# Kernel optimization log

Hardware: AMD Instinct MI355X
Metric: run time of the kernel (lower is better)

The kernel has to match this reference:

```python
import jax, jax.numpy as jnp
import numpy as np
import math

B, S, HID = 2, 2048, 2048
NH, NKV, HD = 16, 4, 128
ROPE_BASE = 10000.0

def _rope(x, position_ids):
    # x: [B, H, S, HD], position_ids: [B, S]
    half = HD // 2
    inv_freq = 1.0 / (ROPE_BASE ** (jnp.arange(0, half, dtype=jnp.float32) / half))
    freqs = position_ids.astype(jnp.float32)[:, :, None] * inv_freq[None, None, :]  # [B,S,half]
    cos = jnp.cos(freqs)[:, None, :, :]  # [B,1,S,half]
    sin = jnp.sin(freqs)[:, None, :, :]
    x1, x2 = x[..., :half], x[..., half:]
    return jnp.concatenate([x1 * cos - x2 * sin, x2 * cos + x1 * sin], axis=-1)

def setup_inputs() -> dict:
    key = jax.random.key(0)
    k1, k2, k3 = jax.random.split(key, 3)
    x = jax.random.normal(k1, (B, S, HID), dtype=jnp.float32)
    position_ids = jnp.broadcast_to(jnp.arange(S, dtype=jnp.int64 if jax.config.jax_enable_x64 else jnp.int32)[None, :], (B, S))
    causal = jnp.tril(jnp.ones((S, S), dtype=bool))
    mask = jnp.where(causal, 0.0, -1e9).astype(jnp.float32)[None, None, :, :]
    w_qkv = jax.random.normal(k2, (NH * HD + 2 * NKV * HD, HID), dtype=jnp.float32) * 0.02
    w_o = jax.random.normal(k3, (HID, HID), dtype=jnp.float32) * 0.02
    return {"x": x, "position_ids": position_ids, "mask": mask, "w_qkv": w_qkv, "w_o": w_o}

def reference(x, position_ids, mask, w_qkv, w_o):
    qkv = x @ w_qkv.T  # [B,S,3072]
    q_dim, kv_dim = NH * HD, NKV * HD
    q = qkv[..., :q_dim].reshape(B, S, NH, HD).transpose(0, 2, 1, 3)          # [B,NH,S,HD]
    k = qkv[..., q_dim:q_dim + kv_dim].reshape(B, S, NKV, HD).transpose(0, 2, 1, 3)
    v = qkv[..., q_dim + kv_dim:].reshape(B, S, NKV, HD).transpose(0, 2, 1, 3)
    q = _rope(q, position_ids)
    k = _rope(k, position_ids)
    n_rep = NH // NKV
    k = jnp.repeat(k, n_rep, axis=1)  # [B,NH,S,HD]
    v = jnp.repeat(v, n_rep, axis=1)
    scores = jnp.einsum('bhqd,bhkd->bhqk', q, k) / math.sqrt(HD) + mask
    attn = jax.nn.softmax(scores, axis=-1)  # dropout p=0.0 -> identity
    out = jnp.einsum('bhqk,bhkd->bhqd', attn, v)
    out = out.transpose(0, 2, 1, 3).reshape(B, S, HID)
    return out @ w_o.T
```

## Files before the change

kernel.cpp:

```cpp
#include <hip/hip_runtime.h>
#include <hip/hip_bf16.h>
#include <cstdint>
#include <cstddef>

typedef unsigned short u16;
typedef __attribute__((ext_vector_type(8))) __bf16 bf16x8;
typedef __attribute__((ext_vector_type(4))) float floatx4;

#define B_    2
#define S_    2048
#define HID_  2048
#define NH_   16
#define NKV_  4
#define HD_   128
#define QKVN_ 3072

__device__ __forceinline__ float bf2f(u16 u) {
  union { unsigned int i; float f; } v; v.i = ((unsigned int)u) << 16; return v.f;
}
__device__ __forceinline__ u16 f2bf(float f) {
  union { float f; unsigned int i; } v; v.f = f;
  unsigned int u = v.i;
  return (u16)((u + 0x7fffu + ((u >> 16) & 1u)) >> 16);
}

#define GLOAD_LDS16(gp, lp)                                                  \
  __builtin_amdgcn_global_load_lds(                                          \
      (__attribute__((address_space(1))) void*)(gp),                         \
      (__attribute__((address_space(3))) void*)(lp), 16, 0, 0)

__global__ __launch_bounds__(256)
void cast_f32_bf16(const float* __restrict__ in, u16* __restrict__ out, int n)
{
  const int i = (blockIdx.x * 256 + threadIdx.x) * 8;
  if (i >= n) return;
  const float4 a = *(const float4*)(in + i);
  const float4 b = *(const float4*)(in + i + 4);
  union { u16 h[8]; uint4 v; } o;
  o.h[0] = f2bf(a.x); o.h[1] = f2bf(a.y); o.h[2] = f2bf(a.z); o.h[3] = f2bf(a.w);
  o.h[4] = f2bf(b.x); o.h[5] = f2bf(b.y); o.h[6] = f2bf(b.z); o.h[7] = f2bf(b.w);
  *(uint4*)(out + i) = o.v;
}

template <bool F32OUT>
__global__ __launch_bounds__(256, 2)
void gemm_bt_128(const u16* __restrict__ A, const u16* __restrict__ W,
                 void* __restrict__ Cv, int N, int K, int lda, int ldc)
{
  __shared__ __align__(16) u16 lA[128 * 64];
  __shared__ __align__(16) u16 lB[128 * 64];
  const int tid  = threadIdx.x;
  const int w    = tid >> 6, ln = tid & 63;
  const int quad = ln >> 4,  l15 = ln & 15;
  const int m0 = blockIdx.y * 128, n0 = blockIdx.x * 128;
  const int waveM = (w >> 1) * 64, waveN = (w & 1) * 64;

  const floatx4 vzero = {0.f, 0.f, 0.f, 0.f};
  floatx4 acc[4][4];
#pragma unroll
  for (int i = 0; i < 4; ++i)
#pragma unroll
    for (int j = 0; j < 4; ++j) acc[i][j] = vzero;

  for (int k0 = 0; k0 < K; k0 += 64) {
    __syncthreads();
#pragma unroll
    for (int p = 0; p < 4; ++p) {
      const int L = (p * 4 + w) * 64 + ln;
      const int row = L >> 3, c = L & 7;
      GLOAD_LDS16(A + (size_t)(m0 + row) * lda + k0 + c * 8, lA + L * 8);
      GLOAD_LDS16(W + (size_t)(n0 + row) * K   + k0 + c * 8, lB + L * 8);
    }
    __syncthreads();
#pragma unroll
    for (int kk = 0; kk < 64; kk += 32) {
      bf16x8 aF[4], bF[4];
      const int cbase = (kk >> 3) + quad;
#pragma unroll
      for (int t = 0; t < 4; ++t) {
        const int rowA = waveM + t * 16 + l15;
        aF[t] = *(const bf16x8*)(lA + rowA * 64 + cbase * 8);
        const int rowB = waveN + t * 16 + l15;
        bF[t] = *(const bf16x8*)(lB + rowB * 64 + cbase * 8);
      }
#pragma unroll
      for (int i = 0; i < 4; ++i)
#pragma unroll
        for (int j = 0; j < 4; ++j)
          acc[i][j] = __builtin_amdgcn_mfma_f32_16x16x32_bf16(aF[i], bF[j], acc[i][j], 0, 0, 0);
    }
  }
#pragma unroll
  for (int i = 0; i < 4; ++i)
#pragma unroll
    for (int r = 0; r < 4; ++r) {
      const int row = m0 + waveM + i * 16 + quad * 4 + r;
      if (F32OUT) {
        float* cp = (float*)Cv + (size_t)row * ldc + n0 + waveN + l15;
#pragma unroll
        for (int j = 0; j < 4; ++j) cp[j * 16] = acc[i][j][r];
      } else {
        u16* cp = (u16*)Cv + (size_t)row * ldc + n0 + waveN + l15;
#pragma unroll
        for (int j = 0; j < 4; ++j) cp[j * 16] = f2bf(acc[i][j][r]);
      }
    }
}

__global__ __launch_bounds__(256)
void rope_inplace(u16* __restrict__ qkv, u16* __restrict__ vt_ws)
{
  const int s = blockIdx.x, b = blockIdx.y;
  const int tid = threadIdx.x;
  __shared__ float cs[64], sn[64];
  if (tid < 64) {
    const float inv = powf(10000.0f, -((float)tid) / 64.0f);
    float s_, c_;
    sincosf((float)s * inv, &s_, &c_);
    cs[tid] = c_; sn[tid] = s_;
  }
  __syncthreads();
  u16* base = qkv + ((size_t)b * S_ + s) * QKVN_;
  for (int p = tid; p < NH_ * 64; p += 256) {
    const int h = p >> 6, i = p & 63;
    u16* hp = base + h * 128;
    const float x1 = bf2f(hp[i]);
    const float x2 = bf2f(hp[64 + i]);
    hp[i]      = f2bf(x1 * cs[i] - x2 * sn[i]);
    hp[64 + i] = f2bf(x2 * cs[i] + x1 * sn[i]);
  }
  for (int p = tid; p < NKV_ * 64; p += 256) {
    const int h = p >> 6, i = p & 63;
    u16* hp = base + NH_ * HD_ + h * 128;
    const float x1 = bf2f(hp[i]);
    const float x2 = bf2f(hp[64 + i]);
    hp[i]      = f2bf(x1 * cs[i] - x2 * sn[i]);
    hp[64 + i] = f2bf(x2 * cs[i] + x1 * sn[i]);
  }
  for (int p = tid; p < NKV_ * HD_; p += 256) {
    const int h = p >> 7, d = p & 127;
    vt_ws[((size_t)(b * NKV_ + h) * HD_ + d) * S_ + s] =
        base[NH_ * HD_ + NKV_ * HD_ + h * 128 + d];
  }
}

#define LPP 68
#define KSLOT(key, s) ((key) * 128 + (((s) ^ ((key) & 7)) * 8))
#define VSLOT(d, s)   ((d) * 64  + (((s) ^ ((d) & 7)) * 8))

__global__ __launch_bounds__(256, 2)
void flash_attn(u16* __restrict__ qkv, const u16* __restrict__ vt_ws)
{
  const int pi = blockIdx.x;
  const int h  = blockIdx.y;
  const int b  = blockIdx.z;
  const int tid  = threadIdx.x;
  const int w    = tid >> 6, ln = tid & 63;
  const int quad = ln >> 4,  l15 = ln & 15;
  const int kvh  = h >> 2;

  const int qtA = 31 - pi, qtB = pi;
  const int itA = qtA + 1;
  const int nIt = itA + qtB + 1;

  __shared__ __align__(16) u16 lK[2][64 * 128];
  __shared__ __align__(16) u16 lVt[2][128 * 64];
  __shared__ __align__(16) u16 lP[4][16 * LPP];

  const float scale = 0.08838834764831845f;
  const u16* kbase = qkv + (size_t)b * S_ * QKVN_ + NH_ * HD_ + kvh * HD_;
  const u16* vbase = vt_ws + (size_t)(b * NKV_ + kvh) * HD_ * S_;
  const floatx4 vzero = {0.f, 0.f, 0.f, 0.f};

  bf16x8 qFA[4], qFB[4];
  {
    const u16* qpA = qkv + ((size_t)(b * S_) + qtA * 64 + w * 16 + l15) * QKVN_ + h * HD_;
    const u16* qpB = qkv + ((size_t)(b * S_) + qtB * 64 + w * 16 + l15) * QKVN_ + h * HD_;
#pragma unroll
    for (int c = 0; c < 4; ++c) {
      qFA[c] = *(const bf16x8*)(qpA + c * 32 + quad * 8);
      qFB[c] = *(const bf16x8*)(qpB + c * 32 + quad * 8);
    }
  }

  float m_i[4], l_i[4];
  floatx4 Oacc[8];
#pragma unroll
  for (int r = 0; r < 4; ++r) { m_i[r] = -1e30f; l_i[r] = 0.f; }
#pragma unroll
  for (int t = 0; t < 8; ++t) Oacc[t] = vzero;

  bf16x8 qF[4];
#pragma unroll
  for (int c = 0; c < 4; ++c) qF[c] = qFA[c];
  int qtC = qtA;
  int qrow0 = qtA * 64 + w * 16;

#pragma unroll
  for (int p = 0; p < 4; ++p) {
    const int idx = (w * 4 + p) * 64 + ln;
    const int key = idx >> 4, ks = idx & 15;
    GLOAD_LDS16(kbase + (size_t)key * QKVN_ + ((ks ^ (key & 7)) * 8),
                lK[0] + (w * 4 + p) * 512);
    const int d = idx >> 3, vs = idx & 7;
    GLOAD_LDS16(vbase + (size_t)d * S_ + ((vs ^ (d & 7)) * 8),
                lVt[0] + (w * 4 + p) * 512);
  }

#pragma unroll 1
  for (int it = 0; it < nIt; ++it) {
    const int ktC = (it < itA) ? it : (it - itA);
    const u16* lKc = lK[it & 1];
    const u16* lVc = lVt[it & 1];
    const bool pf = (it + 1 < nIt);
    if (pf) {
      const int ktN = (it + 1 < itA) ? (it + 1) : (it + 1 - itA);
      u16* lKn = lK[(it + 1) & 1];
      u16* lVn = lVt[(it + 1) & 1];
#pragma unroll
      for (int p = 0; p < 4; ++p) {
        const int idx = (w * 4 + p) * 64 + ln;
        const int key = idx >> 4, ks = idx & 15;
        GLOAD_LDS16(kbase + (size_t)(ktN * 64 + key) * QKVN_ + ((ks ^ (key & 7)) * 8),
                    lKn + (w * 4 + p) * 512);
        const int d = idx >> 3, vs = idx & 7;
        GLOAD_LDS16(vbase + (size_t)d * S_ + ktN * 64 + ((vs ^ (d & 7)) * 8),
                    lVn + (w * 4 + p) * 512);
      }
      asm volatile("s_waitcnt vmcnt(8)" ::: "memory");
    } else {
      asm volatile("s_waitcnt vmcnt(0)" ::: "memory");
    }
    __builtin_amdgcn_s_barrier();
    __builtin_amdgcn_sched_barrier(0);

    floatx4 sc[4];
#pragma unroll
    for (int nt = 0; nt < 4; ++nt) {
      floatx4 a = vzero;
      const int keyloc = nt * 16 + l15;
#pragma unroll
      for (int c = 0; c < 4; ++c) {
        const bf16x8 kF = *(const bf16x8*)(lKc + KSLOT(keyloc, c * 4 + quad));
        a = __builtin_amdgcn_mfma_f32_16x16x32_bf16(qF[c], kF, a, 0, 0, 0);
      }
      sc[nt] = a;
    }

    float pr[4][4];
#pragma unroll
    for (int r = 0; r < 4; ++r) {
      const int qrow = qrow0 + quad * 4 + r;
      float s[4];
#pragma unroll
      for (int nt = 0; nt < 4; ++nt) {
        const int key0 = ktC * 64 + nt * 16 + l15;
        s[nt] = sc[nt][r] * scale + ((key0 <= qrow) ? 0.f : -1e9f);
      }
      float mx = fmaxf(fmaxf(s[0], s[1]), fmaxf(s[2], s[3]));
#pragma unroll
      for (int off = 1; off < 16; off <<= 1) mx = fmaxf(mx, __shfl_xor(mx, off, 64));
      const float mn = fmaxf(m_i[r], mx);
      const float alpha = __expf(m_i[r] - mn);
      float sm = 0.f;
#pragma unroll
      for (int nt = 0; nt < 4; ++nt) {
        const float p = __expf(s[nt] - mn);
        pr[nt][r] = p;
        sm += p;
      }
#pragma unroll
      for (int off = 1; off < 16; off <<= 1) sm += __shfl_xor(sm, off, 64);
      l_i[r] = l_i[r] * alpha + sm;
      m_i[r] = mn;
#pragma unroll
      for (int t = 0; t < 8; ++t) Oacc[t][r] *= alpha;
    }

#pragma unroll
    for (int nt = 0; nt < 4; ++nt)
#pragma unroll
      for (int r = 0; r < 4; ++r)
        lP[w][(quad * 4 + r) * LPP + nt * 16 + l15] = f2bf(pr[nt][r]);

    {
      const bf16x8 pF0 = *(const bf16x8*)(&lP[w][l15 * LPP + quad * 8]);
      const bf16x8 pF1 = *(const bf16x8*)(&lP[w][l15 * LPP + 32 + quad * 8]);
#pragma unroll
      for (int t = 0; t < 8; ++t) {
        const int d = t * 16 + l15;
        const bf16x8 vF0 = *(const bf16x8*)(lVc + VSLOT(d, quad));
        const bf16x8 vF1 = *(const bf16x8*)(lVc + VSLOT(d, 4 + quad));
        Oacc[t] = __builtin_amdgcn_mfma_f32_16x16x32_bf16(pF0, vF0, Oacc[t], 0, 0, 0);
        Oacc[t] = __builtin_amdgcn_mfma_f32_16x16x32_bf16(pF1, vF1, Oacc[t], 0, 0, 0);
      }
    }

    if (ktC == qtC) {
      float linv[4];
#pragma unroll
      for (int r = 0; r < 4; ++r) linv[r] = 1.0f / l_i[r];
#pragma unroll
      for (int t = 0; t < 8; ++t) {
        const int d = t * 16 + l15;
#pragma unroll
        for (int r = 0; r < 4; ++r) {
          const int qrow = qrow0 + quad * 4 + r;
          qkv[((size_t)(b * S_ + qrow)) * QKVN_ + h * HD_ + d] =
              f2bf(Oacc[t][r] * linv[r]);
        }
      }
      if (pf) {
        qtC = qtB;
        qrow0 = qtB * 64 + w * 16;
#pragma unroll
        for (int c = 0; c < 4; ++c) qF[c] = qFB[c];
#pragma unroll
        for (int r = 0; r < 4; ++r) { m_i[r] = -1e30f; l_i[r] = 0.f; }
#pragma unroll
        for (int t = 0; t < 8; ++t) Oacc[t] = vzero;
      }
    }

    __builtin_amdgcn_s_barrier();
  }
}

extern "C" void kernel_launch(void* const* d_in, const int* in_sizes, int n_in,
                              void* d_out, int out_size, void* d_ws, size_t ws_size,
                              hipStream_t stream)
{
  (void)in_sizes; (void)n_in; (void)out_size; (void)ws_size;
  const float* x     = (const float*)d_in[0];
  const float* w_qkv = (const float*)d_in[3];
  const float* w_o   = (const float*)d_in[4];
  float* out = (float*)d_out;

  const int nX  = B_ * S_ * HID_;
  const int nWq = QKVN_ * HID_;
  const int nWo = HID_ * HID_;

  u16* ws    = (u16*)d_ws;
  u16* qkv   = ws;
  u16* slotW = qkv + (size_t)(B_ * S_) * QKVN_;
  u16* xb    = (u16*)d_out;
  u16* vt_ws = (u16*)d_out;

  const dim3 blk(256);
  cast_f32_bf16<<<nX  / 2048, blk, 0, stream>>>(x,     xb,    nX);
  cast_f32_bf16<<<nWq / 2048, blk, 0, stream>>>(w_qkv, slotW, nWq);
  gemm_bt_128<false><<<dim3(QKVN_ / 128, (B_ * S_) / 128), blk, 0, stream>>>(
      xb, slotW, qkv, QKVN_, HID_, HID_, QKVN_);
  rope_inplace<<<dim3(S_, B_), blk, 0, stream>>>(qkv, vt_ws);
  cast_f32_bf16<<<nWo / 2048, blk, 0, stream>>>(w_o, slotW, nWo);
  flash_attn<<<dim3(16, NH_, B_), blk, 0, stream>>>(qkv, vt_ws);
  gemm_bt_128<true><<<dim3(HID_ / 128, (B_ * S_) / 128), blk, 0, stream>>>(
      qkv, slotW, out, HID_, HID_, QKVN_, HID_);
}
```

Measured before the change: 346.8 us.

## Split V transpose into tiled LDS kernel, add MFMA setprio, raise GEMM occupancy

Moves the V transpose out of the RoPE kernel into a dedicated kernel that stages 64x128 tiles in padded shared memory, so both reads and writes are 16-byte vectorized and coalesced. The old path did scattered 2-byte writes strided by S. Also wraps the MFMA sections of flash attention in s_setprio to favour matrix-issuing waves, and raises the GEMM launch-bounds minimum blocks from 2 to 3. This adds an extra kernel launch and may cause register spills in the GEMM.

```diff
diff --git a/kernel.cpp b/kernel.cpp
--- a/kernel.cpp
+++ b/kernel.cpp
@@ -43,7 +43,7 @@
 }
 
 template <bool F32OUT>
-__global__ __launch_bounds__(256, 2)
+__global__ __launch_bounds__(256, 3)
 void gemm_bt_128(const u16* __restrict__ A, const u16* __restrict__ W,
                  void* __restrict__ Cv, int N, int K, int lda, int ldc)
 {
@@ -108,7 +108,7 @@
 }
 
 __global__ __launch_bounds__(256)
-void rope_inplace(u16* __restrict__ qkv, u16* __restrict__ vt_ws)
+void rope_inplace(u16* __restrict__ qkv)
 {
   const int s = blockIdx.x, b = blockIdx.y;
   const int tid = threadIdx.x;
@@ -137,10 +137,40 @@
     hp[i]      = f2bf(x1 * cs[i] - x2 * sn[i]);
     hp[64 + i] = f2bf(x2 * cs[i] + x1 * sn[i]);
   }
-  for (int p = tid; p < NKV_ * HD_; p += 256) {
-    const int h = p >> 7, d = p & 127;
-    vt_ws[((size_t)(b * NKV_ + h) * HD_ + d) * S_ + s] =
-        base[NH_ * HD_ + NKV_ * HD_ + h * 128 + d];
+}
+
+__global__ __launch_bounds__(256)
+void v_transpose(const u16* __restrict__ qkv, u16* __restrict__ vt)
+{
+  const int s0  = blockIdx.x * 64;
+  const int kvh = blockIdx.y;
+  const int b   = blockIdx.z;
+  const int tid = threadIdx.x;
+  __shared__ u16 lT[128 * 73];
+
+  const u16* vsrc = qkv + ((size_t)b * S_ + s0) * QKVN_
+                    + NH_ * HD_ + NKV_ * HD_ + kvh * HD_;
+#pragma unroll
+  for (int p = 0; p < 4; ++p) {
+    const int idx = p * 256 + tid;
+    const int r = idx >> 4, c = idx & 15;
+    union { uint4 v; u16 h[8]; } u;
+    u.v = *(const uint4*)(vsrc + (size_t)r * QKVN_ + c * 8);
+#pragma unroll
+    for (int j = 0; j < 8; ++j)
+      lT[(c * 8 + j) * 73 + r] = u.h[j];
+  }
+  __syncthreads();
+  u16* vdst = vt + ((size_t)(b * NKV_ + kvh) * HD_) * S_ + s0;
+#pragma unroll
+  for (int p = 0; p < 4; ++p) {
+    const int idx = p * 256 + tid;
+    const int d = idx >> 3, rc = idx & 7;
+    union { uint4 v; u16 h[8]; } o;
+#pragma unroll
+    for (int j = 0; j < 8; ++j)
+      o.h[j] = lT[d * 73 + rc * 8 + j];
+    *(uint4*)(vdst + (size_t)d * S_ + rc * 8) = o.v;
   }
 }
 
@@ -235,6 +265,7 @@
     __builtin_amdgcn_sched_barrier(0);
 
     floatx4 sc[4];
+    __builtin_amdgcn_s_setprio(1);
 #pragma unroll
     for (int nt = 0; nt < 4; ++nt) {
       floatx4 a = vzero;
@@ -246,6 +277,7 @@
       }
       sc[nt] = a;
     }
+    __builtin_amdgcn_s_setprio(0);
 
     float pr[4][4];
 #pragma unroll
@@ -286,6 +318,7 @@
     {
       const bf16x8 pF0 = *(const bf16x8*)(&lP[w][l15 * LPP + quad * 8]);
       const bf16x8 pF1 = *(const bf16x8*)(&lP[w][l15 * LPP + 32 + quad * 8]);
+      __builtin_amdgcn_s_setprio(1);
 #pragma unroll
       for (int t = 0; t < 8; ++t) {
         const int d = t * 16 + l15;
@@ -294,6 +327,7 @@
         Oacc[t] = __builtin_amdgcn_mfma_f32_16x16x32_bf16(pF0, vF0, Oacc[t], 0, 0, 0);
         Oacc[t] = __builtin_amdgcn_mfma_f32_16x16x32_bf16(pF1, vF1, Oacc[t], 0, 0, 0);
       }
+      __builtin_amdgcn_s_setprio(0);
     }
 
     if (ktC == qtC) {
@@ -351,7 +385,8 @@
   cast_f32_bf16<<<nWq / 2048, blk, 0, stream>>>(w_qkv, slotW, nWq);
   gemm_bt_128<false><<<dim3(QKVN_ / 128, (B_ * S_) / 128), blk, 0, stream>>>(
       xb, slotW, qkv, QKVN_, HID_, HID_, QKVN_);
-  rope_inplace<<<dim3(S_, B_), blk, 0, stream>>>(qkv, vt_ws);
+  rope_inplace<<<dim3(S_, B_), blk, 0, stream>>>(qkv);
+  v_transpose<<<dim3(S_ / 64, NKV_, B_), blk, 0, stream>>>(qkv, vt_ws);
   cast_f32_bf16<<<nWo / 2048, blk, 0, stream>>>(w_o, slotW, nWo);
   flash_attn<<<dim3(16, NH_, B_), blk, 0, stream>>>(qkv, vt_ws);
   gemm_bt_128<true><<<dim3(HID_ / 128, (B_ * S_) / 128), blk, 0, stream>>>(
```

New measurement: 341.2 us. About the same (-1.6%).
